# Kernel tuning notes

Measured on AMD Instinct MI355X. Metric: run time of the kernel, lower is better.

Reference implementation:

```python
import jax, jax.numpy as jnp
import numpy as np

N_AGENTS = 5
RNN = 128
ATT = 64
N_ACT = 10
IN_DIM = 256
SIZE = 65535  # multiple of N_AGENTS -> padding branch never taken
TAU = 0.01


def _gru_cell(x, h, w_ih, w_hh, b_ih, b_hh):
    # PyTorch GRUCell math
    gi = x @ w_ih.T + b_ih
    gh = h @ w_hh.T + b_hh
    i_r, i_z, i_n = jnp.split(gi, 3, axis=-1)
    h_r, h_z, h_n = jnp.split(gh, 3, axis=-1)
    r = jax.nn.sigmoid(i_r + h_r)
    z = jax.nn.sigmoid(i_z + h_z)
    n = jnp.tanh(i_n + r * h_n)
    return (1.0 - z) * n + z * h


def _gru_seq(xs, w_ih, w_hh, b_ih, b_hh):
    # xs: [T, B, D]; zero initial hidden, returns all step outputs [T, B, RNN]
    h0 = jnp.zeros((xs.shape[1], RNN), xs.dtype)
    def step(h, x):
        h2 = _gru_cell(x, h, w_ih, w_hh, b_ih, b_hh)
        return h2, h2
    _, ys = jax.lax.scan(step, h0, xs)
    return ys


def setup_inputs():
    key = jax.random.key(0)
    ks = jax.random.split(key, 26)
    def u(k, shape, fan):
        return jax.random.uniform(k, shape, jnp.float32, -1.0, 1.0) / np.sqrt(fan)
    return {
        'obs': jax.random.normal(ks[0], (SIZE, IN_DIM), jnp.float32),
        'hidden_state': jax.random.normal(ks[1], (SIZE, RNN), jnp.float32),
        'enc_w': u(ks[2], (RNN, IN_DIM), IN_DIM), 'enc_b': u(ks[3], (RNN,), IN_DIM),
        'gru_w_ih': u(ks[4], (3 * RNN, RNN), RNN), 'gru_w_hh': u(ks[5], (3 * RNN, RNN), RNN),
        'gru_b_ih': u(ks[6], (3 * RNN,), RNN), 'gru_b_hh': u(ks[7], (3 * RNN,), RNN),
        'bi_w_ih_f': u(ks[8], (3 * RNN, 2 * RNN), RNN), 'bi_w_hh_f': u(ks[9], (3 * RNN, RNN), RNN),
        'bi_b_ih_f': u(ks[10], (3 * RNN,), RNN), 'bi_b_hh_f': u(ks[11], (3 * RNN,), RNN),
        'bi_w_ih_r': u(ks[12], (3 * RNN, 2 * RNN), RNN), 'bi_w_hh_r': u(ks[13], (3 * RNN, RNN), RNN),
        'bi_b_ih_r': u(ks[14], (3 * RNN,), RNN), 'bi_b_hh_r': u(ks[15], (3 * RNN,), RNN),
        'hard_w': u(ks[16], (2, 2 * RNN), 2 * RNN), 'hard_b': u(ks[17], (2,), 2 * RNN),
        'q_w': u(ks[18], (ATT, RNN), RNN),
        'k_w': u(ks[19], (ATT, RNN), RNN),
        'v_w': u(ks[20], (ATT, RNN), RNN), 'v_b': u(ks[21], (ATT,), RNN),
        'dec_w': u(ks[22], (N_ACT, RNN + ATT), RNN + ATT), 'dec_b': u(ks[23], (N_ACT,), RNN + ATT),
    }


def reference(obs, hidden_state, enc_w, enc_b, gru_w_ih, gru_w_hh, gru_b_ih, gru_b_hh,
              bi_w_ih_f, bi_w_hh_f, bi_b_ih_f, bi_b_hh_f,
              bi_w_ih_r, bi_w_hh_r, bi_b_ih_r, bi_b_hh_r,
              hard_w, hard_b, q_w, k_w, v_w, v_b, dec_w, dec_b):
    size = obs.shape[0]
    bpa = size // N_AGENTS  # batch per agent; SIZE is a multiple of N_AGENTS

    x = jax.nn.relu(obs @ enc_w.T + enc_b)
    h_out = _gru_cell(x, hidden_state, gru_w_ih, gru_w_hh, gru_b_ih, gru_b_hh)

    # --- hard attention: pairwise agent features -> bi-GRU -> gumbel-softmax gate ---
    # (computed exactly as in the original; note the original soft_attention
    #  ignores hard_weights, so this does not influence the returned output)
    h = h_out.reshape(bpa, N_AGENTS, RNN)
    nbr = np.array([[j for j in range(N_AGENTS) if j != i] for i in range(N_AGENTS)])  # [n, n-1]
    h_i = jnp.broadcast_to(h[:, :, None, :], (bpa, N_AGENTS, N_AGENTS - 1, RNN))
    h_j = h[:, nbr, :]                              # [bpa, n, n-1, RNN]
    pair = jnp.concatenate([h_i, h_j], axis=-1)     # [bpa, n, n-1, 2*RNN]
    seq = pair.transpose(2, 0, 1, 3).reshape(N_AGENTS - 1, bpa * N_AGENTS, 2 * RNN)
    fwd = _gru_seq(seq, bi_w_ih_f, bi_w_hh_f, bi_b_ih_f, bi_b_hh_f)
    bwd = _gru_seq(seq[::-1], bi_w_ih_r, bi_w_hh_r, bi_b_ih_r, bi_b_hh_r)[::-1]
    h_hard = jnp.concatenate([fwd, bwd], axis=-1)   # [n-1, B, 2*RNN]
    h_hard = h_hard.transpose(1, 0, 2).reshape(-1, 2 * RNN)
    logits = h_hard @ hard_w.T + hard_b             # [B*(n-1), 2]
    u01 = jax.random.uniform(jax.random.key(42), logits.shape, jnp.float32, 1e-10, 1.0)
    gumbel = -jnp.log(-jnp.log(u01))
    gs = jax.nn.softmax((logits + gumbel) / TAU, axis=-1)
    hard_weights = gs[:, 1].reshape(bpa, N_AGENTS, 1, N_AGENTS - 1).transpose(1, 0, 2, 3)
    _ = hard_weights  # unused downstream, matching the original module

    # --- soft attention: original loops per sample doing a 1x1 matmul+softmax;
    #     vectorized here. softmax over a single element is identically 1. ---
    q = h_out @ q_w.T
    k = h_out @ k_w.T
    v = jax.nn.relu(h_out @ v_w.T + v_b)
    score = jnp.sum(q * k, axis=-1, keepdims=True) / np.sqrt(ATT)  # [B,1]
    soft_w = jax.nn.softmax(score, axis=-1)                         # all ones
    x_att = v * soft_w

    final_input = jnp.concatenate([h_out, x_att], axis=-1)
    output = final_input @ dec_w.T + dec_b
    return output, h_out
```

## Files before the change

### kernel.cpp

```cpp
#include <hip/hip_runtime.h>
#include <stdint.h>

#define SIZE 65535

typedef __bf16 bf16x8 __attribute__((ext_vector_type(8)));
typedef float floatx4 __attribute__((ext_vector_type(4)));

#define WS_ENCW 0
#define WS_WIH  32768
#define WS_WHH  81920
#define WS_VW   131072
#define WS_DECW 139264
#define WS_TOTC 17920
#define X_WS    143360

__device__ __forceinline__ unsigned short f2bf(float f) {
    union { float f; unsigned int u; } v; v.f = f;
    unsigned int u = v.u;
    return (unsigned short)((u + 0x7fffu + ((u >> 16) & 1u)) >> 16);
}
__device__ __forceinline__ float sigmf(float x) {
    x = fminf(fmaxf(x, -30.f), 30.f);
    return 1.f / (1.f + __expf(-x));
}
__device__ __forceinline__ float tanhfast(float x) {
    x = fminf(fmaxf(x, -15.f), 15.f);
    float e = __expf(2.f * x);
    return (e - 1.f) / (e + 1.f);
}

union BF8 { bf16x8 v; unsigned short s[8]; };

__device__ __forceinline__ bf16x8 cvt8g(const float* p) {
    float4 a = *reinterpret_cast<const float4*>(p);
    float4 b = *reinterpret_cast<const float4*>(p + 4);
    BF8 r;
    r.s[0] = f2bf(a.x); r.s[1] = f2bf(a.y); r.s[2] = f2bf(a.z); r.s[3] = f2bf(a.w);
    r.s[4] = f2bf(b.x); r.s[5] = f2bf(b.y); r.s[6] = f2bf(b.z); r.s[7] = f2bf(b.w);
    return r.v;
}
__device__ __forceinline__ bf16x8 ld8(const unsigned short* p) {
    return *reinterpret_cast<const bf16x8*>(p);
}
__device__ __forceinline__ void glds16(const unsigned short* g, unsigned short* l) {
    __builtin_amdgcn_global_load_lds(
        (const __attribute__((address_space(1))) unsigned int*)g,
        (__attribute__((address_space(3))) unsigned int*)l, 16, 0, 0);
}

__global__ __launch_bounds__(256) void cvt_weights(
    const float* __restrict__ enc_w, const float* __restrict__ w_ih,
    const float* __restrict__ w_hh, const float* __restrict__ v_w,
    const float* __restrict__ dec_w, unsigned short* __restrict__ ws) {
    int c = blockIdx.x * 256 + threadIdx.x;
    if (c >= WS_TOTC) return;
    const int lane = c & 63;
    const int l = lane & 15;
    const int q = lane >> 4;
    const float* src; int row, col, stride; bool zero = false;
    if (c < 4096) {
        int lt = c >> 6; int nt = lt >> 3, kt = lt & 7;
        row = nt * 16 + l; col = kt * 32 + q * 8; src = enc_w; stride = 256;
    } else if (c < 10240) {
        int lt = (c - 4096) >> 6; int nt = lt / 12; int r2 = lt % 12;
        int g = r2 >> 2, kt = r2 & 3;
        row = g * 128 + nt * 16 + l; col = kt * 32 + q * 8; src = w_ih; stride = 128;
    } else if (c < 16384) {
        int lt = (c - 10240) >> 6; int nt = lt / 12; int r2 = lt % 12;
        int g = r2 >> 2, kt = r2 & 3;
        row = g * 128 + nt * 16 + l; col = kt * 32 + q * 8; src = w_hh; stride = 128;
    } else if (c < 17408) {
        int lt = (c - 16384) >> 6; int nt = lt >> 2, kt = lt & 3;
        row = nt * 16 + l; col = kt * 32 + q * 8; src = v_w; stride = 128;
    } else {
        int kt = (c - 17408) >> 6;
        row = l; col = kt * 32 + q * 8; src = dec_w; stride = 192;
        zero = (l >= 10) || (kt >= 6);
    }
    float4 a, b;
    if (zero) { a = make_float4(0.f,0.f,0.f,0.f); b = a; }
    else {
        const float* p = src + (size_t)row * stride + col;
        a = *reinterpret_cast<const float4*>(p);
        b = *reinterpret_cast<const float4*>(p + 4);
    }
    unsigned short* d = ws + (size_t)c * 8;
    d[0]=f2bf(a.x); d[1]=f2bf(a.y); d[2]=f2bf(a.z); d[3]=f2bf(a.w);
    d[4]=f2bf(b.x); d[5]=f2bf(b.y); d[6]=f2bf(b.z); d[7]=f2bf(b.w);
}

__global__ __launch_bounds__(256, 2) void pass1_enc(
    const float* __restrict__ obs,
    const float* __restrict__ enc_b,
    const unsigned short* __restrict__ wsw,
    unsigned short* __restrict__ xws)
{
    __shared__ __align__(16) unsigned short wenc[32768];

    const int tid  = threadIdx.x;
    const int wave = tid >> 6;
    const int lane = tid & 63;
    const int l15  = lane & 15;
    const int quad = lane >> 4;
    const int wrow0 = blockIdx.x * 128 + wave * 32;

#pragma unroll
    for (int s = 0; s < 16; ++s) {
        const int c = s * 256 + tid;
        glds16(wsw + WS_ENCW + (size_t)c * 8, wenc + (size_t)c * 8);
    }

    int rA0 = wrow0 + l15;      rA0 = (rA0 < SIZE) ? rA0 : (SIZE - 1);
    int rA1 = wrow0 + 16 + l15; rA1 = (rA1 < SIZE) ? rA1 : (SIZE - 1);

    bf16x8 bo[2][8];
    {
        const float* o0 = obs + (size_t)rA0 * 256;
        const float* o1 = obs + (size_t)rA1 * 256;
#pragma unroll
        for (int kt = 0; kt < 8; ++kt) {
            bo[0][kt] = cvt8g(o0 + kt * 32 + quad * 8);
            bo[1][kt] = cvt8g(o1 + kt * 32 + quad * 8);
        }
    }
    __syncthreads();

#pragma unroll 1
    for (int nt = 0; nt < 8; ++nt) {
        floatx4 d0 = floatx4{0.f,0.f,0.f,0.f}, d1 = d0;
#pragma unroll
        for (int kt = 0; kt < 8; ++kt) {
            bf16x8 a = ld8(&wenc[(nt * 8 + kt) * 512 + lane * 8]);
            d0 = __builtin_amdgcn_mfma_f32_16x16x32_bf16(a, bo[0][kt], d0, 0, 0, 0);
            d1 = __builtin_amdgcn_mfma_f32_16x16x32_bf16(a, bo[1][kt], d1, 0, 0, 0);
        }
        const float4 ebv = *reinterpret_cast<const float4*>(enc_b + nt * 16 + quad * 4);
        const float eb[4] = {ebv.x, ebv.y, ebv.z, ebv.w};
#pragma unroll
        for (int m = 0; m < 2; ++m) {
            const int grow = wrow0 + m * 16 + l15;
            if (grow < SIZE) {
                const floatx4& d = m ? d1 : d0;
                ushort4 pk;
                pk.x = f2bf(fmaxf(d[0] + eb[0], 0.f));
                pk.y = f2bf(fmaxf(d[1] + eb[1], 0.f));
                pk.z = f2bf(fmaxf(d[2] + eb[2], 0.f));
                pk.w = f2bf(fmaxf(d[3] + eb[3], 0.f));
                *reinterpret_cast<ushort4*>(xws + (size_t)grow * 128 + nt * 16 + quad * 4) = pk;
            }
        }
    }
}

__global__ __launch_bounds__(256, 3) void pass2_gru(
    const float* __restrict__ hid,
    const float* __restrict__ b_ih,
    const float* __restrict__ b_hh,
    const unsigned short* __restrict__ wsw,
    const unsigned short* __restrict__ xws,
    float* __restrict__ out_h)
{
    __shared__ __align__(16) unsigned short wq[24576];

    const int tid  = threadIdx.x;
    const int wave = tid >> 6;
    const int lane = tid & 63;
    const int l15  = lane & 15;
    const int quad = lane >> 4;
    const int q    = blockIdx.x & 3;
    const int tile = blockIdx.x >> 2;
    const int wrow0 = tile * 128 + wave * 32;

#pragma unroll
    for (int s = 0; s < 12; ++s) {
        const int c = s * 256 + tid;
        const int f = c >> 6, li = c & 63;
        int ff = (f < 24) ? f : f - 24;
        const int ntL = ff / 12, rm = ff % 12;
        const int g = rm >> 2, kt = rm & 3;
        const int gidx = (((q * 2 + ntL) * 3 + g) * 4 + kt);
        const unsigned short* src = wsw + ((f < 24) ? WS_WIH : WS_WHH)
                                        + (size_t)gidx * 512 + li * 8;
        glds16(src, wq + (size_t)c * 8);
    }

    int rA0 = wrow0 + l15;      rA0 = (rA0 < SIZE) ? rA0 : (SIZE - 1);
    int rA1 = wrow0 + 16 + l15; rA1 = (rA1 < SIZE) ? rA1 : (SIZE - 1);

    bf16x8 xb[2][4], hb[2][4];
#pragma unroll
    for (int kt = 0; kt < 4; ++kt) {
        xb[0][kt] = ld8(xws + (size_t)rA0 * 128 + kt * 32 + quad * 8);
        xb[1][kt] = ld8(xws + (size_t)rA1 * 128 + kt * 32 + quad * 8);
        hb[0][kt] = cvt8g(hid + (size_t)rA0 * 128 + kt * 32 + quad * 8);
        hb[1][kt] = cvt8g(hid + (size_t)rA1 * 128 + kt * 32 + quad * 8);
    }
    __syncthreads();

#pragma unroll 1
    for (int ntL = 0; ntL < 2; ++ntL) {
        const int oc0 = q * 32 + ntL * 16;
        floatx4 gi[3][2], gh[3][2];
#pragma unroll
        for (int g = 0; g < 3; ++g) {
            gi[g][0] = floatx4{0.f,0.f,0.f,0.f}; gi[g][1] = gi[g][0];
            gh[g][0] = gi[g][0]; gh[g][1] = gi[g][0];
        }
#pragma unroll
        for (int g = 0; g < 3; ++g)
#pragma unroll
            for (int kt = 0; kt < 4; ++kt) {
                bf16x8 ai = ld8(&wq[((ntL * 3 + g) * 4 + kt) * 512 + lane * 8]);
                bf16x8 ah = ld8(&wq[12288 + ((ntL * 3 + g) * 4 + kt) * 512 + lane * 8]);
                gi[g][0] = __builtin_amdgcn_mfma_f32_16x16x32_bf16(ai, xb[0][kt], gi[g][0], 0, 0, 0);
                gi[g][1] = __builtin_amdgcn_mfma_f32_16x16x32_bf16(ai, xb[1][kt], gi[g][1], 0, 0, 0);
                gh[g][0] = __builtin_amdgcn_mfma_f32_16x16x32_bf16(ah, hb[0][kt], gh[g][0], 0, 0, 0);
                gh[g][1] = __builtin_amdgcn_mfma_f32_16x16x32_bf16(ah, hb[1][kt], gh[g][1], 0, 0, 0);
            }
        const float4 birv = *reinterpret_cast<const float4*>(b_ih + oc0 + quad * 4);
        const float4 bizv = *reinterpret_cast<const float4*>(b_ih + 128 + oc0 + quad * 4);
        const float4 binv = *reinterpret_cast<const float4*>(b_ih + 256 + oc0 + quad * 4);
        const float4 bhrv = *reinterpret_cast<const float4*>(b_hh + oc0 + quad * 4);
        const float4 bhzv = *reinterpret_cast<const float4*>(b_hh + 128 + oc0 + quad * 4);
        const float4 bhnv = *reinterpret_cast<const float4*>(b_hh + 256 + oc0 + quad * 4);
        const float bir[4] = {birv.x, birv.y, birv.z, birv.w};
        const float biz[4] = {bizv.x, bizv.y, bizv.z, bizv.w};
        const float bin[4] = {binv.x, binv.y, binv.z, binv.w};
        const float bhr[4] = {bhrv.x, bhrv.y, bhrv.z, bhrv.w};
        const float bhz[4] = {bhzv.x, bhzv.y, bhzv.z, bhzv.w};
        const float bhn[4] = {bhnv.x, bhnv.y, bhnv.z, bhnv.w};
#pragma unroll
        for (int m = 0; m < 2; ++m) {
            const int grow = wrow0 + m * 16 + l15;
            const int rowc = (grow < SIZE) ? grow : (SIZE - 1);
            const float4 hpv = *reinterpret_cast<const float4*>(hid + (size_t)rowc * 128 + oc0 + quad * 4);
            const float hp[4] = {hpv.x, hpv.y, hpv.z, hpv.w};
            float ho[4];
#pragma unroll
            for (int r = 0; r < 4; ++r) {
                float rg = sigmf(gi[0][m][r] + bir[r] + gh[0][m][r] + bhr[r]);
                float zg = sigmf(gi[1][m][r] + biz[r] + gh[1][m][r] + bhz[r]);
                float ng = tanhfast(gi[2][m][r] + bin[r] + rg * (gh[2][m][r] + bhn[r]));
                ho[r] = (1.f - zg) * ng + zg * hp[r];
            }
            if (grow < SIZE)
                *reinterpret_cast<float4*>(out_h + (size_t)grow * 128 + oc0 + quad * 4) =
                    make_float4(ho[0], ho[1], ho[2], ho[3]);
        }
    }
}

__global__ __launch_bounds__(256, 3) void pass3_vdec(
    const float* __restrict__ hsrc,
    const float* __restrict__ v_b,
    const float* __restrict__ dec_b,
    const unsigned short* __restrict__ wsw,
    float* __restrict__ out)
{
    __shared__ __align__(16) unsigned short wv[8192];
    __shared__ __align__(16) unsigned short wdec[4096];
    __shared__ __align__(16) unsigned short sV[4][32][72];
    __shared__ __align__(16) float sO[4][32][10];

    const int tid  = threadIdx.x;
    const int wave = tid >> 6;
    const int lane = tid & 63;
    const int l15  = lane & 15;
    const int quad = lane >> 4;
    const int wrow0 = blockIdx.x * 128 + wave * 32;

#pragma unroll
    for (int s = 0; s < 4; ++s) {
        const int c = s * 256 + tid;
        glds16(wsw + WS_VW + (size_t)c * 8, wv + (size_t)c * 8);
    }
#pragma unroll
    for (int s = 0; s < 2; ++s) {
        const int c = s * 256 + tid;
        glds16(wsw + WS_DECW + (size_t)c * 8, wdec + (size_t)c * 8);
    }

    int rA0 = wrow0 + l15;      rA0 = (rA0 < SIZE) ? rA0 : (SIZE - 1);
    int rA1 = wrow0 + 16 + l15; rA1 = (rA1 < SIZE) ? rA1 : (SIZE - 1);

    bf16x8 ha[2][4];
#pragma unroll
    for (int kt = 0; kt < 4; ++kt) {
        ha[0][kt] = cvt8g(hsrc + (size_t)rA0 * 128 + kt * 32 + quad * 8);
        ha[1][kt] = cvt8g(hsrc + (size_t)rA1 * 128 + kt * 32 + quad * 8);
    }
    __syncthreads();

#pragma unroll 1
    for (int nt = 0; nt < 4; ++nt) {
        floatx4 a0 = floatx4{0.f,0.f,0.f,0.f}, a1 = a0;
#pragma unroll
        for (int kt = 0; kt < 4; ++kt) {
            bf16x8 b = ld8(&wv[(nt * 4 + kt) * 512 + lane * 8]);
            a0 = __builtin_amdgcn_mfma_f32_16x16x32_bf16(ha[0][kt], b, a0, 0, 0, 0);
            a1 = __builtin_amdgcn_mfma_f32_16x16x32_bf16(ha[1][kt], b, a1, 0, 0, 0);
        }
        const float bias = v_b[nt * 16 + l15];
#pragma unroll
        for (int r = 0; r < 4; ++r) {
            sV[wave][quad * 4 + r][nt * 16 + l15]      = f2bf(fmaxf(a0[r] + bias, 0.f));
            sV[wave][16 + quad * 4 + r][nt * 16 + l15] = f2bf(fmaxf(a1[r] + bias, 0.f));
        }
    }

    {
        floatx4 d0 = floatx4{0.f,0.f,0.f,0.f}, d1 = d0;
#pragma unroll
        for (int kt = 0; kt < 6; ++kt) {
            bf16x8 b = ld8(&wdec[kt * 512 + lane * 8]);
            bf16x8 a0 = (kt < 4) ? ha[0][kt] : ld8(&sV[wave][l15][(kt - 4) * 32 + quad * 8]);
            bf16x8 a1 = (kt < 4) ? ha[1][kt] : ld8(&sV[wave][16 + l15][(kt - 4) * 32 + quad * 8]);
            d0 = __builtin_amdgcn_mfma_f32_16x16x32_bf16(a0, b, d0, 0, 0, 0);
            d1 = __builtin_amdgcn_mfma_f32_16x16x32_bf16(a1, b, d1, 0, 0, 0);
        }
        if (l15 < 10) {
            const float bias = dec_b[l15];
#pragma unroll
            for (int r = 0; r < 4; ++r) {
                sO[wave][quad * 4 + r][l15]      = d0[r] + bias;
                sO[wave][16 + quad * 4 + r][l15] = d1[r] + bias;
            }
        }
#pragma unroll
        for (int j = 0; j < 5; ++j) {
            int idx = j * 64 + lane;
            int row = idx / 10, col = idx % 10;
            int grow = wrow0 + row;
            if (grow < SIZE)
                out[(size_t)grow * 10 + col] = sO[wave][row][col];
        }
    }
}

extern "C" void kernel_launch(void* const* d_in, const int* in_sizes, int n_in,
                              void* d_out, int out_size, void* d_ws, size_t ws_size,
                              hipStream_t stream) {
    const float* obs   = (const float*)d_in[0];
    const float* hid   = (const float*)d_in[1];
    const float* enc_w = (const float*)d_in[2];
    const float* enc_b = (const float*)d_in[3];
    const float* w_ih  = (const float*)d_in[4];
    const float* w_hh  = (const float*)d_in[5];
    const float* b_ih  = (const float*)d_in[6];
    const float* b_hh  = (const float*)d_in[7];
    const float* v_w   = (const float*)d_in[20];
    const float* v_b   = (const float*)d_in[21];
    const float* dec_w = (const float*)d_in[22];
    const float* dec_b = (const float*)d_in[23];
    unsigned short* wsw = (unsigned short*)d_ws;
    unsigned short* xws = wsw + X_WS;
    float* out   = (float*)d_out;
    float* out_h = out + (size_t)SIZE * 10;

    hipLaunchKernelGGL(cvt_weights, dim3((WS_TOTC + 255) / 256), dim3(256), 0, stream,
                       enc_w, w_ih, w_hh, v_w, dec_w, wsw);
    hipLaunchKernelGGL(pass1_enc, dim3(512), dim3(256), 0, stream,
                       obs, enc_b, wsw, xws);
    hipLaunchKernelGGL(pass2_gru, dim3(2048), dim3(256), 0, stream,
                       hid, b_ih, b_hh, wsw, xws, out_h);
    hipLaunchKernelGGL(pass3_vdec, dim3(512), dim3(256), 0, stream,
                       out_h, v_b, dec_b, wsw, out);
}
```

Before: 234.4 us.

## Split encoder output columns across blocks and swizzle block IDs per XCD

The encoder pass now splits its 128 output columns into two halves across twice as many blocks. Each block stages only half the encoder weights in LDS, which allows higher occupancy through launch bounds. Block IDs in the encoder and GRU passes are remapped so that blocks sharing a row tile land on the same XCD, aiming for better L2 reuse of obs/hidden rows. The GRU epilogue is fully unrolled and defers its stores to the end. The trade-off is that each obs row is loaded twice in pass1 and register pressure in pass2 goes up.

```diff
diff --git a/kernel.cpp b/kernel.cpp
--- a/kernel.cpp
+++ b/kernel.cpp
@@ -89,25 +89,30 @@
     d[4]=f2bf(b.x); d[5]=f2bf(b.y); d[6]=f2bf(b.z); d[7]=f2bf(b.w);
 }
 
-__global__ __launch_bounds__(256, 2) void pass1_enc(
+__global__ __launch_bounds__(256, 4) void pass1_enc(
     const float* __restrict__ obs,
     const float* __restrict__ enc_b,
     const unsigned short* __restrict__ wsw,
     unsigned short* __restrict__ xws)
 {
-    __shared__ __align__(16) unsigned short wenc[32768];
+    __shared__ __align__(16) unsigned short wenc[16384];
 
     const int tid  = threadIdx.x;
     const int wave = tid >> 6;
     const int lane = tid & 63;
     const int l15  = lane & 15;
     const int quad = lane >> 4;
-    const int wrow0 = blockIdx.x * 128 + wave * 32;
-
-#pragma unroll
-    for (int s = 0; s < 16; ++s) {
-        const int c = s * 256 + tid;
-        glds16(wsw + WS_ENCW + (size_t)c * 8, wenc + (size_t)c * 8);
+    const int b    = blockIdx.x;
+    const int xcd  = b & 7;
+    const int s    = b >> 3;
+    const int tile = xcd * 64 + (s >> 1);
+    const int half = s & 1;
+    const int wrow0 = tile * 128 + wave * 32;
+
+#pragma unroll
+    for (int st = 0; st < 8; ++st) {
+        const int c = st * 256 + tid;
+        glds16(wsw + WS_ENCW + half * 16384 + (size_t)c * 8, wenc + (size_t)c * 8);
     }
 
     int rA0 = wrow0 + l15;      rA0 = (rA0 < SIZE) ? rA0 : (SIZE - 1);
@@ -126,15 +131,16 @@
     __syncthreads();
 
 #pragma unroll 1
-    for (int nt = 0; nt < 8; ++nt) {
+    for (int ntl = 0; ntl < 4; ++ntl) {
         floatx4 d0 = floatx4{0.f,0.f,0.f,0.f}, d1 = d0;
 #pragma unroll
         for (int kt = 0; kt < 8; ++kt) {
-            bf16x8 a = ld8(&wenc[(nt * 8 + kt) * 512 + lane * 8]);
+            bf16x8 a = ld8(&wenc[(ntl * 8 + kt) * 512 + lane * 8]);
             d0 = __builtin_amdgcn_mfma_f32_16x16x32_bf16(a, bo[0][kt], d0, 0, 0, 0);
             d1 = __builtin_amdgcn_mfma_f32_16x16x32_bf16(a, bo[1][kt], d1, 0, 0, 0);
         }
-        const float4 ebv = *reinterpret_cast<const float4*>(enc_b + nt * 16 + quad * 4);
+        const int col0 = half * 64 + ntl * 16 + quad * 4;
+        const float4 ebv = *reinterpret_cast<const float4*>(enc_b + col0);
         const float eb[4] = {ebv.x, ebv.y, ebv.z, ebv.w};
 #pragma unroll
         for (int m = 0; m < 2; ++m) {
@@ -146,7 +152,7 @@
                 pk.y = f2bf(fmaxf(d[1] + eb[1], 0.f));
                 pk.z = f2bf(fmaxf(d[2] + eb[2], 0.f));
                 pk.w = f2bf(fmaxf(d[3] + eb[3], 0.f));
-                *reinterpret_cast<ushort4*>(xws + (size_t)grow * 128 + nt * 16 + quad * 4) = pk;
+                *reinterpret_cast<ushort4*>(xws + (size_t)grow * 128 + col0) = pk;
             }
         }
     }
@@ -167,13 +173,16 @@
     const int lane = tid & 63;
     const int l15  = lane & 15;
     const int quad = lane >> 4;
-    const int q    = blockIdx.x & 3;
-    const int tile = blockIdx.x >> 2;
+    const int b    = blockIdx.x;
+    const int xcd  = b & 7;
+    const int s    = b >> 3;
+    const int tile = xcd * 64 + (s >> 2);
+    const int q    = s & 3;
     const int wrow0 = tile * 128 + wave * 32;
 
 #pragma unroll
-    for (int s = 0; s < 12; ++s) {
-        const int c = s * 256 + tid;
+    for (int st = 0; st < 12; ++st) {
+        const int c = st * 256 + tid;
         const int f = c >> 6, li = c & 63;
         int ff = (f < 24) ? f : f - 24;
         const int ntL = ff / 12, rm = ff % 12;
@@ -197,9 +206,10 @@
     }
     __syncthreads();
 
-#pragma unroll 1
+    float ho[2][2][4];
+#pragma unroll
     for (int ntL = 0; ntL < 2; ++ntL) {
-        const int oc0 = q * 32 + ntL * 16;
+        const int oc0 = q * 32 + ntL * 16 + quad * 4;
         floatx4 gi[3][2], gh[3][2];
 #pragma unroll
         for (int g = 0; g < 3; ++g) {
@@ -217,12 +227,12 @@
                 gh[g][0] = __builtin_amdgcn_mfma_f32_16x16x32_bf16(ah, hb[0][kt], gh[g][0], 0, 0, 0);
                 gh[g][1] = __builtin_amdgcn_mfma_f32_16x16x32_bf16(ah, hb[1][kt], gh[g][1], 0, 0, 0);
             }
-        const float4 birv = *reinterpret_cast<const float4*>(b_ih + oc0 + quad * 4);
-        const float4 bizv = *reinterpret_cast<const float4*>(b_ih + 128 + oc0 + quad * 4);
-        const float4 binv = *reinterpret_cast<const float4*>(b_ih + 256 + oc0 + quad * 4);
-        const float4 bhrv = *reinterpret_cast<const float4*>(b_hh + oc0 + quad * 4);
-        const float4 bhzv = *reinterpret_cast<const float4*>(b_hh + 128 + oc0 + quad * 4);
-        const float4 bhnv = *reinterpret_cast<const float4*>(b_hh + 256 + oc0 + quad * 4);
+        const float4 birv = *reinterpret_cast<const float4*>(b_ih + oc0);
+        const float4 bizv = *reinterpret_cast<const float4*>(b_ih + 128 + oc0);
+        const float4 binv = *reinterpret_cast<const float4*>(b_ih + 256 + oc0);
+        const float4 bhrv = *reinterpret_cast<const float4*>(b_hh + oc0);
+        const float4 bhzv = *reinterpret_cast<const float4*>(b_hh + 128 + oc0);
+        const float4 bhnv = *reinterpret_cast<const float4*>(b_hh + 256 + oc0);
         const float bir[4] = {birv.x, birv.y, birv.z, birv.w};
         const float biz[4] = {bizv.x, bizv.y, bizv.z, bizv.w};
         const float bin[4] = {binv.x, binv.y, binv.z, binv.w};
@@ -233,19 +243,27 @@
         for (int m = 0; m < 2; ++m) {
             const int grow = wrow0 + m * 16 + l15;
             const int rowc = (grow < SIZE) ? grow : (SIZE - 1);
-            const float4 hpv = *reinterpret_cast<const float4*>(hid + (size_t)rowc * 128 + oc0 + quad * 4);
+            const float4 hpv = *reinterpret_cast<const float4*>(hid + (size_t)rowc * 128 + oc0);
             const float hp[4] = {hpv.x, hpv.y, hpv.z, hpv.w};
-            float ho[4];
 #pragma unroll
             for (int r = 0; r < 4; ++r) {
                 float rg = sigmf(gi[0][m][r] + bir[r] + gh[0][m][r] + bhr[r]);
                 float zg = sigmf(gi[1][m][r] + biz[r] + gh[1][m][r] + bhz[r]);
                 float ng = tanhfast(gi[2][m][r] + bin[r] + rg * (gh[2][m][r] + bhn[r]));
-                ho[r] = (1.f - zg) * ng + zg * hp[r];
-            }
-            if (grow < SIZE)
-                *reinterpret_cast<float4*>(out_h + (size_t)grow * 128 + oc0 + quad * 4) =
-                    make_float4(ho[0], ho[1], ho[2], ho[3]);
+                ho[ntL][m][r] = (1.f - zg) * ng + zg * hp[r];
+            }
+        }
+    }
+#pragma unroll
+    for (int m = 0; m < 2; ++m) {
+        const int grow = wrow0 + m * 16 + l15;
+        if (grow < SIZE) {
+#pragma unroll
+            for (int ntL = 0; ntL < 2; ++ntL) {
+                const int oc0 = q * 32 + ntL * 16 + quad * 4;
+                *reinterpret_cast<float4*>(out_h + (size_t)grow * 128 + oc0) =
+                    make_float4(ho[ntL][m][0], ho[ntL][m][1], ho[ntL][m][2], ho[ntL][m][3]);
+            }
         }
     }
 }
@@ -270,13 +288,13 @@
     const int wrow0 = blockIdx.x * 128 + wave * 32;
 
 #pragma unroll
-    for (int s = 0; s < 4; ++s) {
-        const int c = s * 256 + tid;
+    for (int st = 0; st < 4; ++st) {
+        const int c = st * 256 + tid;
         glds16(wsw + WS_VW + (size_t)c * 8, wv + (size_t)c * 8);
     }
 #pragma unroll
-    for (int s = 0; s < 2; ++s) {
-        const int c = s * 256 + tid;
+    for (int st = 0; st < 2; ++st) {
+        const int c = st * 256 + tid;
         glds16(wsw + WS_DECW + (size_t)c * 8, wdec + (size_t)c * 8);
     }
 
@@ -359,7 +377,7 @@
 
     hipLaunchKernelGGL(cvt_weights, dim3((WS_TOTC + 255) / 256), dim3(256), 0, stream,
                        enc_w, w_ih, w_hh, v_w, dec_w, wsw);
-    hipLaunchKernelGGL(pass1_enc, dim3(512), dim3(256), 0, stream,
+    hipLaunchKernelGGL(pass1_enc, dim3(1024), dim3(256), 0, stream,
                        obs, enc_b, wsw, xws);
     hipLaunchKernelGGL(pass2_gru, dim3(2048), dim3(256), 0, stream,
                        hid, b_ih, b_hh, wsw, xws, out_h);
```

New measurement: 251.0 us. +7.1%, slower.
